# Performance work log

Measured on AMD Instinct MI355X. Metric: run time of the kernel, lower is better.

Reference implementation:

```python
import jax, jax.numpy as jnp
import numpy as np

N_NODES = 50000
N_EDGES = 800000
D_MODEL = 128
N_HEAD = 8
D_HEAD = D_MODEL // N_HEAD  # 16
D_FF = 2 * D_MODEL
EPS = 1e-5


def _layer_norm(x, g=None, b=None):
    mu = jnp.mean(x, axis=-1, keepdims=True)
    var = jnp.mean((x - mu) ** 2, axis=-1, keepdims=True)
    y = (x - mu) * jax.lax.rsqrt(var + EPS)
    if g is not None:
        y = y * g + b
    return y


def setup_inputs() -> dict:
    key = jax.random.key(0)
    ks = jax.random.split(key, 14)
    w = lambda k, shp: jax.random.normal(k, shp, dtype=jnp.float32) * 0.05
    return {
        "bond_embedding": jax.random.normal(ks[0], (N_EDGES, D_MODEL), dtype=jnp.float32),
        "node_embedding": jax.random.normal(ks[1], (N_NODES, D_MODEL), dtype=jnp.float32),
        "basic_attn": jax.random.uniform(ks[2], (N_EDGES, 1), dtype=jnp.float32),
        "Wk": w(ks[3], (D_MODEL, D_MODEL)),
        "Wq": w(ks[4], (D_MODEL, D_MODEL)),
        "Wv": w(ks[5], (D_MODEL, D_MODEL)),
        "W_dis": w(ks[6], (N_HEAD, 1)),
        "W_beta": w(ks[7], (1, 3 * D_MODEL)),
        "W1": w(ks[8], (D_FF, D_MODEL)),
        "W2": w(ks[9], (D_MODEL, D_FF)),
        "ln1_g": jnp.ones((D_MODEL,), dtype=jnp.float32),
        "ln1_b": jnp.zeros((D_MODEL,), dtype=jnp.float32),
        "src": jax.random.randint(ks[10], (N_EDGES,), 0, N_NODES, dtype=jnp.int32),
        "dst": jax.random.randint(ks[11], (N_EDGES,), 0, N_NODES, dtype=jnp.int32),
    }


def reference(bond_embedding, node_embedding, basic_attn, Wk, Wq, Wv, W_dis,
              W_beta, W1, W2, ln1_g, ln1_b, src, dst):
    # projections -> per-head layout
    v = (bond_embedding @ Wv.T).reshape(N_EDGES, N_HEAD, D_HEAD)  # edge values
    k = (node_embedding @ Wk.T).reshape(N_NODES, N_HEAD, D_HEAD)
    q = (node_embedding @ Wq.T).reshape(N_NODES, N_HEAD, D_HEAD)

    # u_dot_v('k','q'): per-edge per-head dot product, scaled by sqrt(d_head)
    att = jnp.einsum("ehd,ehd->eh", k[src], q[dst]) / jnp.sqrt(jnp.float32(D_HEAD))
    # distance-decay bias: Linear(1 -> num_head) on per-edge scalar
    logits = att + basic_attn @ W_dis.T  # [E, H]

    # edge_softmax over incoming edges of each dst node (per head)
    m = jax.ops.segment_max(logits, dst, num_segments=N_NODES)
    m = jnp.where(jnp.isfinite(m), m, 0.0)  # isolated nodes
    p = jnp.exp(logits - m[dst])
    s = jax.ops.segment_sum(p, dst, num_segments=N_NODES)
    a = p / s[dst]  # [E, H]

    # weighted scatter-sum of edge values to dst nodes
    ft = jax.ops.segment_sum(v * a[..., None], dst, num_segments=N_NODES)
    he = ft.reshape(N_NODES, D_MODEL)

    # beta gating
    beta = jax.nn.sigmoid(
        jnp.concatenate([he, node_embedding, he - node_embedding], axis=-1) @ W_beta.T
    )  # [N, 1]
    he = beta * node_embedding + (1.0 - beta) * he

    # PoswiseFeedForwardNet: LN -> FFN -> residual -> fresh (non-affine) LN
    residual = he
    h = _layer_norm(he, ln1_g, ln1_b)
    h = jax.nn.relu(h @ W1.T) @ W2.T
    return _layer_norm(h + residual)
```

## Files before the change

kernel.cpp:

```cpp
#include <hip/hip_runtime.h>
#include <hip/hip_bf16.h>

#define N_NODES 50000
#define N_EDGES 800000
#define D 128
#define NH 8
#define DH 16
#define DFF 256
#define LN_EPS 1e-5f
#define GN 16
#define NPB 32
#define SCAN_BS 512
#define NSCAN ((N_NODES + SCAN_BS - 1) / SCAN_BS)

typedef __attribute__((ext_vector_type(8))) short bf16x8;
typedef __attribute__((ext_vector_type(8))) unsigned short u16x8;
typedef __attribute__((ext_vector_type(4))) float f32x4;
typedef unsigned short ushort_t;

__device__ __forceinline__ float wred(float v) {
#pragma unroll
    for (int o = 32; o; o >>= 1) v += __shfl_xor(v, o);
    return v;
}

__device__ __forceinline__ short f2b(float f) {
    unsigned u = __float_as_uint(f);
    unsigned r = u + 0x7fffu + ((u >> 16) & 1u);
    return (short)(r >> 16);
}
__device__ __forceinline__ float b2f(unsigned short u) {
    return __uint_as_float((unsigned)u << 16);
}

__global__ __launch_bounds__(256) void k_zero(int* __restrict__ p) {
    int i = blockIdx.x * 256 + threadIdx.x;
    if (i < N_NODES) p[i] = 0;
}

__global__ __launch_bounds__(128) void k_qkproj(
    const float* __restrict__ x, const float* __restrict__ Wk,
    const float* __restrict__ Wq, ushort_t* __restrict__ kout,
    ushort_t* __restrict__ qout) {
    __shared__ float xs[16][128];
    const int t = threadIdx.x;
    const int nb = blockIdx.x * 16;
#pragma unroll
    for (int r = 0; r < 16; ++r) xs[r][t] = x[(size_t)(nb + r) * D + t];
    __syncthreads();
    const float4* wk4 = (const float4*)(Wk + (size_t)t * D);
    const float4* wq4 = (const float4*)(Wq + (size_t)t * D);
    float ka[16] = {}, qa[16] = {};
#pragma unroll 4
    for (int i4 = 0; i4 < 32; ++i4) {
        float4 wk = wk4[i4], wq = wq4[i4];
#pragma unroll
        for (int r = 0; r < 16; ++r) {
            float4 xv = *(const float4*)&xs[r][i4 * 4];
            ka[r] += wk.x * xv.x + wk.y * xv.y + wk.z * xv.z + wk.w * xv.w;
            qa[r] += wq.x * xv.x + wq.y * xv.y + wq.z * xv.z + wq.w * xv.w;
        }
    }
#pragma unroll
    for (int r = 0; r < 16; ++r) {
        kout[(size_t)(nb + r) * D + t] = (ushort_t)f2b(ka[r]);
        qout[(size_t)(nb + r) * D + t] = (ushort_t)f2b(qa[r]);
    }
}

__global__ __launch_bounds__(256) void k_hist(const int* __restrict__ dst,
                                              int* __restrict__ deg) {
    int e = blockIdx.x * 256 + threadIdx.x;
    atomicAdd(&deg[dst[e]], 1);
}

__global__ __launch_bounds__(SCAN_BS) void k_scan1(
    const int* __restrict__ deg, int* __restrict__ scanout,
    int* __restrict__ bsum) {
    __shared__ int ss[SCAN_BS];
    const int t = threadIdx.x;
    const int i = blockIdx.x * SCAN_BS + t;
    int v = (i < N_NODES) ? deg[i] : 0;
    ss[t] = v;
    __syncthreads();
    for (int off = 1; off < SCAN_BS; off <<= 1) {
        int a = (t >= off) ? ss[t - off] : 0;
        __syncthreads();
        ss[t] += a;
        __syncthreads();
    }
    if (i < N_NODES) scanout[i] = ss[t] - v;
    if (t == SCAN_BS - 1) bsum[blockIdx.x] = ss[t];
}

__global__ __launch_bounds__(128) void k_scan2(int* __restrict__ bsum) {
    __shared__ int ss[128];
    const int t = threadIdx.x;
    int v = (t < NSCAN) ? bsum[t] : 0;
    ss[t] = v;
    __syncthreads();
    for (int off = 1; off < 128; off <<= 1) {
        int a = (t >= off) ? ss[t - off] : 0;
        __syncthreads();
        ss[t] += a;
        __syncthreads();
    }
    if (t < NSCAN) bsum[t] = ss[t] - v;
}

__global__ __launch_bounds__(256) void k_scan3(
    const int* __restrict__ scanout, const int* __restrict__ bsum,
    int* __restrict__ rowstart, int* __restrict__ cursor) {
    int i = blockIdx.x * 256 + threadIdx.x;
    if (i < N_NODES) {
        int rs = scanout[i] + bsum[i / SCAN_BS];
        rowstart[i] = rs;
        cursor[i] = rs;
    }
    if (i == 0) rowstart[N_NODES] = N_EDGES;
}

__global__ __launch_bounds__(256) void k_fill(const int* __restrict__ dst,
                                              int* __restrict__ cursor,
                                              int* __restrict__ eidx) {
    int e = blockIdx.x * 256 + threadIdx.x;
    int pos = atomicAdd(&cursor[dst[e]], 1);
    eidx[pos] = e;
}

__global__ __launch_bounds__(256) void k_attn(
    const ushort_t* __restrict__ kv, const ushort_t* __restrict__ qv,
    const float* __restrict__ basic, const float* __restrict__ Wdis,
    const int* __restrict__ src, const int* __restrict__ rowstart,
    const int* __restrict__ eidx, float* __restrict__ aperm) {
    const int t = threadIdx.x;
    const int lane = t & 63, wv = t >> 6;
    const int n = blockIdx.x * 4 + wv;
    const int j = lane >> 3, h = lane & 7;
    const int rs = rowstart[n], re = rowstart[n + 1];
    const float wd = Wdis[h];
    const ushort_t* qp = qv + (size_t)n * D + h * DH;
    u16x8 q0 = *(const u16x8*)qp;
    u16x8 q1 = *(const u16x8*)(qp + 8);
    float qf[16];
#pragma unroll
    for (int i = 0; i < 8; ++i) { qf[i] = b2f(q0[i]); qf[8 + i] = b2f(q1[i]); }

    float ml = -1e30f;
    for (int base = rs; base < re; base += 8) {
        int pos = base + j;
        float l = -1e30f;
        if (pos < re) {
            int e = eidx[pos];
            int sc = src[e];
            const ushort_t* kp = kv + (size_t)sc * D + h * DH;
            u16x8 k0 = *(const u16x8*)kp;
            u16x8 k1 = *(const u16x8*)(kp + 8);
            float acc = 0.f;
#pragma unroll
            for (int i = 0; i < 8; ++i) acc += qf[i] * b2f(k0[i]);
#pragma unroll
            for (int i = 0; i < 8; ++i) acc += qf[8 + i] * b2f(k1[i]);
            l = acc * 0.25f + basic[e] * wd;
            aperm[(size_t)pos * NH + h] = l;
        }
        ml = fmaxf(ml, l);
    }
    ml = fmaxf(ml, __shfl_xor(ml, 8));
    ml = fmaxf(ml, __shfl_xor(ml, 16));
    ml = fmaxf(ml, __shfl_xor(ml, 32));
    float sl = 0.f;
    for (int base = rs; base < re; base += 8) {
        int pos = base + j;
        if (pos < re) {
            float p = expf(aperm[(size_t)pos * NH + h] - ml);
            aperm[(size_t)pos * NH + h] = p;
            sl += p;
        }
    }
    sl += __shfl_xor(sl, 8);
    sl += __shfl_xor(sl, 16);
    sl += __shfl_xor(sl, 32);
    float siv = (sl > 0.f) ? 1.f / sl : 0.f;
    for (int base = rs; base < re; base += 8) {
        int pos = base + j;
        if (pos < re) aperm[(size_t)pos * NH + h] *= siv;
    }
}

__global__ __launch_bounds__(256) void k_hsum(
    const float* __restrict__ bond, const float* __restrict__ Wv,
    const float* __restrict__ aperm, const int* __restrict__ rowstart,
    const int* __restrict__ eidx, float* __restrict__ ft) {
    __shared__ short slds[8 * 16 * 128];
    __shared__ int srs[GN + 1];
    const int t = threadIdx.x;
    const int lane = t & 63, w = t >> 6;
    const int lr = lane & 15, lg = lane >> 4;
    const int n0 = blockIdx.x * GN;
    if (t < GN + 1) srs[t] = rowstart[n0 + t];
    __syncthreads();

    const int c0 = lane * 2;
    const int chunk = lane >> 2;
    const int elo = (lane * 2) & 7;

#pragma unroll
    for (int i = 0; i < 4; ++i) {
        int ln = w + i * 4;
        int rs = srs[ln], re = srs[ln + 1];
        float sacc[8][2];
#pragma unroll
        for (int h = 0; h < 8; ++h) { sacc[h][0] = 0.f; sacc[h][1] = 0.f; }
        int pos = rs;
        for (; pos + 2 <= re; pos += 2) {
            int e0 = eidx[pos], e1 = eidx[pos + 1];
            float2 b0 = *(const float2*)&bond[(size_t)e0 * D + c0];
            float2 b1 = *(const float2*)&bond[(size_t)e1 * D + c0];
            float4 a00 = *(const float4*)&aperm[(size_t)pos * 8];
            float4 a01 = *(const float4*)&aperm[(size_t)pos * 8 + 4];
            float4 a10 = *(const float4*)&aperm[(size_t)(pos + 1) * 8];
            float4 a11 = *(const float4*)&aperm[(size_t)(pos + 1) * 8 + 4];
            const float a0v[8] = {a00.x, a00.y, a00.z, a00.w,
                                  a01.x, a01.y, a01.z, a01.w};
            const float a1v[8] = {a10.x, a10.y, a10.z, a10.w,
                                  a11.x, a11.y, a11.z, a11.w};
#pragma unroll
            for (int h = 0; h < 8; ++h) {
                sacc[h][0] += a0v[h] * b0.x + a1v[h] * b1.x;
                sacc[h][1] += a0v[h] * b0.y + a1v[h] * b1.y;
            }
        }
        for (; pos < re; ++pos) {
            int e = eidx[pos];
            float2 b = *(const float2*)&bond[(size_t)e * D + c0];
            float4 a0 = *(const float4*)&aperm[(size_t)pos * 8];
            float4 a1 = *(const float4*)&aperm[(size_t)pos * 8 + 4];
            const float av[8] = {a0.x, a0.y, a0.z, a0.w,
                                 a1.x, a1.y, a1.z, a1.w};
#pragma unroll
            for (int h = 0; h < 8; ++h) {
                sacc[h][0] += av[h] * b.x;
                sacc[h][1] += av[h] * b.y;
            }
        }
#pragma unroll
        for (int h = 0; h < 8; ++h) {
            unsigned u = (unsigned)(unsigned short)f2b(sacc[h][0]) |
                         ((unsigned)(unsigned short)f2b(sacc[h][1]) << 16);
            *(unsigned*)&slds[(h * 16 + ln) * 128 +
                              ((chunk ^ (ln & 7)) << 3) + elo] = u;
        }
    }
    __syncthreads();

    bf16x8 bfr[2][4];
#pragma unroll
    for (int nn = 0; nn < 2; ++nn) {
        int col = (2 * w + nn) * 16 + lr;
#pragma unroll
        for (int ks = 0; ks < 4; ++ks) {
            const float4* gp = (const float4*)(Wv + (size_t)col * D + ks * 32 + lg * 8);
            float4 f0 = gp[0], f1 = gp[1];
            bf16x8 v;
            v[0] = f2b(f0.x); v[1] = f2b(f0.y); v[2] = f2b(f0.z); v[3] = f2b(f0.w);
            v[4] = f2b(f1.x); v[5] = f2b(f1.y); v[6] = f2b(f1.z); v[7] = f2b(f1.w);
            bfr[nn][ks] = v;
        }
    }
    f32x4 acc[2];
#pragma unroll
    for (int nn = 0; nn < 2; ++nn) acc[nn] = (f32x4){0.f, 0.f, 0.f, 0.f};
#pragma unroll
    for (int ks = 0; ks < 4; ++ks) {
        int ck = ks * 4 + lg;
#pragma unroll
        for (int nn = 0; nn < 2; ++nn) {
            int h = 2 * w + nn;
            bf16x8 sf = *(const bf16x8*)&slds[(h * 16 + lr) * 128 +
                                              ((ck ^ (lr & 7)) << 3)];
            acc[nn] = __builtin_amdgcn_mfma_f32_16x16x32_bf16(
                bfr[nn][ks], sf, acc[nn], 0, 0, 0);
        }
    }
#pragma unroll
    for (int nn = 0; nn < 2; ++nn) {
        float4 o = {acc[nn][0], acc[nn][1], acc[nn][2], acc[nn][3]};
        *(float4*)&ft[(size_t)(n0 + lr) * D + (2 * w + nn) * 16 + lg * 4] = o;
    }
}

__global__ __launch_bounds__(256, 2) void k_node(
    const float* __restrict__ ft, const float* __restrict__ x,
    const float* __restrict__ Wb, const float* __restrict__ W1,
    const float* __restrict__ W2, const float* __restrict__ g_ln,
    const float* __restrict__ b_ln, float* __restrict__ out) {
    __shared__ float hs[NPB][132];
    __shared__ short hA[NPB * 128];
    __shared__ short hid[NPB * 256];
    __shared__ float ylds[NPB][132];
    const int t = threadIdx.x;
    const int lane = t & 63, w = t >> 6;
    const int lr = lane & 15, lg = lane >> 4;
    const int n0 = blockIdx.x * NPB;
    const int c0 = lane * 2;

    const float2 wb0 = *(const float2*)&Wb[c0];
    const float2 wb1 = *(const float2*)&Wb[128 + c0];
    const float2 wb2 = *(const float2*)&Wb[256 + c0];
    const float2 gv = *(const float2*)&g_ln[c0];
    const float2 bv = *(const float2*)&b_ln[c0];
#pragma unroll
    for (int i = 0; i < 8; ++i) {
        int n = w * 8 + i;
        int gn = n0 + n;
        float2 fv = {0.f, 0.f}, xv = {0.f, 0.f};
        if (gn < N_NODES) {
            fv = *(const float2*)&ft[(size_t)gn * D + c0];
            xv = *(const float2*)&x[(size_t)gn * D + c0];
        }
        float part = fv.x * wb0.x + fv.y * wb0.y + xv.x * wb1.x + xv.y * wb1.y +
                     (fv.x - xv.x) * wb2.x + (fv.y - xv.y) * wb2.y;
        float beta = 1.f / (1.f + expf(-wred(part)));
        float hex = beta * xv.x + (1.f - beta) * fv.x;
        float hey = beta * xv.y + (1.f - beta) * fv.y;
        hs[n][c0] = hex;
        hs[n][c0 + 1] = hey;
        float mu = wred(hex + hey) * (1.f / 128.f);
        float dx = hex - mu, dy = hey - mu;
        float var = wred(dx * dx + dy * dy) * (1.f / 128.f);
        float rs = rsqrtf(var + LN_EPS);
        float h0 = dx * rs * gv.x + bv.x;
        float h1 = dy * rs * gv.y + bv.y;
        unsigned u = (unsigned)(unsigned short)f2b(h0) |
                     ((unsigned)(unsigned short)f2b(h1) << 16);
        int phys = (lane >> 2) ^ (n & 7);
        ((unsigned*)hA)[n * 64 + phys * 4 + (lane & 3)] = u;
    }
    __syncthreads();

    {
        bf16x8 b1[4][4];
#pragma unroll
        for (int nt = 0; nt < 4; ++nt) {
            int col = w * 64 + nt * 16 + lr;
#pragma unroll
            for (int ks = 0; ks < 4; ++ks) {
                const float4* gp = (const float4*)(W1 + (size_t)col * D + ks * 32 + lg * 8);
                float4 f0 = gp[0], f1 = gp[1];
                bf16x8 v;
                v[0] = f2b(f0.x); v[1] = f2b(f0.y); v[2] = f2b(f0.z); v[3] = f2b(f0.w);
                v[4] = f2b(f1.x); v[5] = f2b(f1.y); v[6] = f2b(f1.z); v[7] = f2b(f1.w);
                b1[nt][ks] = v;
            }
        }
        f32x4 acc1[2][4];
#pragma unroll
        for (int m = 0; m < 2; ++m)
#pragma unroll
            for (int nt = 0; nt < 4; ++nt) acc1[m][nt] = (f32x4){0.f, 0.f, 0.f, 0.f};
#pragma unroll
        for (int ks = 0; ks < 4; ++ks) {
            int chunk = ks * 4 + lg;
#pragma unroll
            for (int m = 0; m < 2; ++m) {
                int row = m * 16 + lr;
                bf16x8 af = *(const bf16x8*)&hA[row * 128 + ((chunk ^ (row & 7)) << 3)];
#pragma unroll
                for (int nt = 0; nt < 4; ++nt)
                    acc1[m][nt] = __builtin_amdgcn_mfma_f32_16x16x32_bf16(
                        af, b1[nt][ks], acc1[m][nt], 0, 0, 0);
            }
        }
#pragma unroll
        for (int m = 0; m < 2; ++m)
#pragma unroll
            for (int nt = 0; nt < 4; ++nt)
#pragma unroll
                for (int r = 0; r < 4; ++r) {
                    int node = m * 16 + lg * 4 + r;
                    int col = w * 64 + nt * 16 + lr;
                    float v = fmaxf(acc1[m][nt][r], 0.f);
                    hid[node * 256 + (((col >> 3) ^ (node & 7)) << 3) + (col & 7)] = f2b(v);
                }
    }
    __syncthreads();

    {
        bf16x8 b2[2][8];
#pragma unroll
        for (int nt = 0; nt < 2; ++nt) {
            int col = w * 32 + nt * 16 + lr;
#pragma unroll
            for (int ks = 0; ks < 8; ++ks) {
                const float4* gp = (const float4*)(W2 + (size_t)col * DFF + ks * 32 + lg * 8);
                float4 f0 = gp[0], f1 = gp[1];
                bf16x8 v;
                v[0] = f2b(f0.x); v[1] = f2b(f0.y); v[2] = f2b(f0.z); v[3] = f2b(f0.w);
                v[4] = f2b(f1.x); v[5] = f2b(f1.y); v[6] = f2b(f1.z); v[7] = f2b(f1.w);
                b2[nt][ks] = v;
            }
        }
        f32x4 acc2[2][2];
#pragma unroll
        for (int m = 0; m < 2; ++m)
#pragma unroll
            for (int nt = 0; nt < 2; ++nt) acc2[m][nt] = (f32x4){0.f, 0.f, 0.f, 0.f};
#pragma unroll
        for (int ks = 0; ks < 8; ++ks) {
            int chunk = ks * 4 + lg;
#pragma unroll
            for (int m = 0; m < 2; ++m) {
                int row = m * 16 + lr;
                bf16x8 af = *(const bf16x8*)&hid[row * 256 + ((chunk ^ (row & 7)) << 3)];
#pragma unroll
                for (int nt = 0; nt < 2; ++nt)
                    acc2[m][nt] = __builtin_amdgcn_mfma_f32_16x16x32_bf16(
                        af, b2[nt][ks], acc2[m][nt], 0, 0, 0);
            }
        }
#pragma unroll
        for (int m = 0; m < 2; ++m)
#pragma unroll
            for (int nt = 0; nt < 2; ++nt)
#pragma unroll
                for (int r = 0; r < 4; ++r) {
                    int node = m * 16 + lg * 4 + r;
                    int col = w * 32 + nt * 16 + lr;
                    ylds[node][col] = acc2[m][nt][r] + hs[node][col];
                }
    }
    __syncthreads();

#pragma unroll
    for (int i = 0; i < 8; ++i) {
        int n = w * 8 + i;
        int gn = n0 + n;
        float y0 = ylds[n][c0], y1 = ylds[n][c0 + 1];
        float mu = wred(y0 + y1) * (1.f / 128.f);
        float d0 = y0 - mu, d1 = y1 - mu;
        float var = wred(d0 * d0 + d1 * d1) * (1.f / 128.f);
        float rs = rsqrtf(var + LN_EPS);
        if (gn < N_NODES) {
            float2 o = {d0 * rs, d1 * rs};
            *(float2*)&out[(size_t)gn * D + c0] = o;
        }
    }
}

extern "C" void kernel_launch(void* const* d_in, const int* in_sizes, int n_in,
                              void* d_out, int out_size, void* d_ws, size_t ws_size,
                              hipStream_t stream) {
    const float* bond = (const float*)d_in[0];
    const float* x    = (const float*)d_in[1];
    const float* basic= (const float*)d_in[2];
    const float* Wk   = (const float*)d_in[3];
    const float* Wq   = (const float*)d_in[4];
    const float* Wv   = (const float*)d_in[5];
    const float* Wdis = (const float*)d_in[6];
    const float* Wb   = (const float*)d_in[7];
    const float* W1   = (const float*)d_in[8];
    const float* W2   = (const float*)d_in[9];
    const float* g_ln = (const float*)d_in[10];
    const float* b_ln = (const float*)d_in[11];
    const int* src    = (const int*)d_in[12];
    const int* dst    = (const int*)d_in[13];
    float* out = (float*)d_out;

    ushort_t* kbf = (ushort_t*)d_ws;
    ushort_t* qbf = kbf + (size_t)N_NODES * D;
    float* aperm = (float*)(qbf + (size_t)N_NODES * D);
    float* ftb   = aperm + (size_t)N_EDGES * NH;
    int* deg     = (int*)(ftb + (size_t)N_NODES * D);
    int* scanout = deg + N_NODES;
    int* bsum    = scanout + N_NODES;
    int* rowstart= bsum + 128;
    int* cursor  = rowstart + N_NODES + 1;
    int* eidx    = cursor + N_NODES;

    k_zero<<<(N_NODES + 255) / 256, 256, 0, stream>>>(deg);
    k_qkproj<<<N_NODES / 16, 128, 0, stream>>>(x, Wk, Wq, kbf, qbf);
    k_hist<<<N_EDGES / 256, 256, 0, stream>>>(dst, deg);
    k_scan1<<<NSCAN, SCAN_BS, 0, stream>>>(deg, scanout, bsum);
    k_scan2<<<1, 128, 0, stream>>>(bsum);
    k_scan3<<<(N_NODES + 255) / 256, 256, 0, stream>>>(scanout, bsum, rowstart, cursor);
    k_fill<<<N_EDGES / 256, 256, 0, stream>>>(dst, cursor, eidx);
    k_attn<<<N_NODES / 4, 256, 0, stream>>>(kbf, qbf, basic, Wdis, src,
                                            rowstart, eidx, aperm);
    k_hsum<<<N_NODES / GN, 256, 0, stream>>>(bond, Wv, aperm, rowstart, eidx, ftb);
    k_node<<<(N_NODES + NPB - 1) / NPB, 256, 0, stream>>>(ftb, x, Wb, W1, W2,
                                                          g_ln, b_ln, out);
}
```

Baseline: 538.2 us.

## Drop softmax max pass and defer normalization into aggregation kernel

```diff
diff --git a/kernel.cpp b/kernel.cpp
--- a/kernel.cpp
+++ b/kernel.cpp
@@ -132,7 +132,8 @@
     const ushort_t* __restrict__ kv, const ushort_t* __restrict__ qv,
     const float* __restrict__ basic, const float* __restrict__ Wdis,
     const int* __restrict__ src, const int* __restrict__ rowstart,
-    const int* __restrict__ eidx, float* __restrict__ aperm) {
+    const int* __restrict__ eidx, float* __restrict__ aperm,
+    float* __restrict__ sinv) {
     const int t = threadIdx.x;
     const int lane = t & 63, wv = t >> 6;
     const int n = blockIdx.x * 4 + wv;
@@ -146,10 +147,9 @@
 #pragma unroll
     for (int i = 0; i < 8; ++i) { qf[i] = b2f(q0[i]); qf[8 + i] = b2f(q1[i]); }
 
-    float ml = -1e30f;
+    float sl = 0.f;
     for (int base = rs; base < re; base += 8) {
         int pos = base + j;
-        float l = -1e30f;
         if (pos < re) {
             int e = eidx[pos];
             int sc = src[e];
@@ -161,19 +161,7 @@
             for (int i = 0; i < 8; ++i) acc += qf[i] * b2f(k0[i]);
 #pragma unroll
             for (int i = 0; i < 8; ++i) acc += qf[8 + i] * b2f(k1[i]);
-            l = acc * 0.25f + basic[e] * wd;
-            aperm[(size_t)pos * NH + h] = l;
-        }
-        ml = fmaxf(ml, l);
-    }
-    ml = fmaxf(ml, __shfl_xor(ml, 8));
-    ml = fmaxf(ml, __shfl_xor(ml, 16));
-    ml = fmaxf(ml, __shfl_xor(ml, 32));
-    float sl = 0.f;
-    for (int base = rs; base < re; base += 8) {
-        int pos = base + j;
-        if (pos < re) {
-            float p = expf(aperm[(size_t)pos * NH + h] - ml);
+            float p = expf(acc * 0.25f + basic[e] * wd);
             aperm[(size_t)pos * NH + h] = p;
             sl += p;
         }
@@ -181,24 +169,23 @@
     sl += __shfl_xor(sl, 8);
     sl += __shfl_xor(sl, 16);
     sl += __shfl_xor(sl, 32);
-    float siv = (sl > 0.f) ? 1.f / sl : 0.f;
-    for (int base = rs; base < re; base += 8) {
-        int pos = base + j;
-        if (pos < re) aperm[(size_t)pos * NH + h] *= siv;
-    }
+    if (lane < 8) sinv[(size_t)n * NH + h] = (sl > 0.f) ? 1.f / sl : 0.f;
 }
 
 __global__ __launch_bounds__(256) void k_hsum(
     const float* __restrict__ bond, const float* __restrict__ Wv,
-    const float* __restrict__ aperm, const int* __restrict__ rowstart,
-    const int* __restrict__ eidx, float* __restrict__ ft) {
+    const float* __restrict__ aperm, const float* __restrict__ sinv,
+    const int* __restrict__ rowstart, const int* __restrict__ eidx,
+    float* __restrict__ ft) {
     __shared__ short slds[8 * 16 * 128];
+    __shared__ float sivlds[GN * 8];
     __shared__ int srs[GN + 1];
     const int t = threadIdx.x;
     const int lane = t & 63, w = t >> 6;
     const int lr = lane & 15, lg = lane >> 4;
     const int n0 = blockIdx.x * GN;
     if (t < GN + 1) srs[t] = rowstart[n0 + t];
+    if (t < GN * 8) sivlds[t] = sinv[(size_t)n0 * 8 + t];
     __syncthreads();
 
     const int c0 = lane * 2;
@@ -246,8 +233,9 @@
         }
 #pragma unroll
         for (int h = 0; h < 8; ++h) {
-            unsigned u = (unsigned)(unsigned short)f2b(sacc[h][0]) |
-                         ((unsigned)(unsigned short)f2b(sacc[h][1]) << 16);
+            float siv = sivlds[ln * 8 + h];
+            unsigned u = (unsigned)(unsigned short)f2b(sacc[h][0] * siv) |
+                         ((unsigned)(unsigned short)f2b(sacc[h][1] * siv) << 16);
             *(unsigned*)&slds[(h * 16 + ln) * 128 +
                               ((chunk ^ (ln & 7)) << 3) + elo] = u;
         }
@@ -471,7 +459,8 @@
     ushort_t* qbf = kbf + (size_t)N_NODES * D;
     float* aperm = (float*)(qbf + (size_t)N_NODES * D);
     float* ftb   = aperm + (size_t)N_EDGES * NH;
-    int* deg     = (int*)(ftb + (size_t)N_NODES * D);
+    float* sinvb = ftb + (size_t)N_NODES * D;
+    int* deg     = (int*)(sinvb + (size_t)N_NODES * NH);
     int* scanout = deg + N_NODES;
     int* bsum    = scanout + N_NODES;
     int* rowstart= bsum + 128;
@@ -486,8 +475,9 @@
     k_scan3<<<(N_NODES + 255) / 256, 256, 0, stream>>>(scanout, bsum, rowstart, cursor);
     k_fill<<<N_EDGES / 256, 256, 0, stream>>>(dst, cursor, eidx);
     k_attn<<<N_NODES / 4, 256, 0, stream>>>(kbf, qbf, basic, Wdis, src,
-                                            rowstart, eidx, aperm);
-    k_hsum<<<N_NODES / GN, 256, 0, stream>>>(bond, Wv, aperm, rowstart, eidx, ftb);
+                                            rowstart, eidx, aperm, sinvb);
+    k_hsum<<<N_NODES / GN, 256, 0, stream>>>(bond, Wv, aperm, sinvb,
+                                             rowstart, eidx, ftb);
     k_node<<<(N_NODES + NPB - 1) / NPB, 256, 0, stream>>>(ftb, x, Wb, W1, W2,
                                                           g_ln, b_ln, out);
 }
```

After: 521.8 us. 1.03x faster.
